# Kernel tuning notes

Hardware: AMD Instinct MI355X
Metric: run time of the kernel (lower is better)

## Reference

```python
import jax, jax.numpy as jnp
import numpy as np

N_SRC = 50000
N_DST = 10000
E = 1600000
H = 1
F = 128
NEG_SLOPE = 0.2  # GAT default leaky_relu slope


def setup_inputs() -> dict:
    key = jax.random.key(0)
    k1, k2, k3, k4, k5, k6 = jax.random.split(key, 6)
    x_src = jax.random.normal(k1, (N_SRC, H, F), dtype=jnp.float32)
    x_dst = jax.random.normal(k2, (N_DST, H, F), dtype=jnp.float32)
    attn_l = jax.random.normal(k3, (1, H, F), dtype=jnp.float32)
    attn_r = jax.random.normal(k4, (1, H, F), dtype=jnp.float32)
    src_idx = jax.random.randint(k5, (E,), 0, N_SRC, dtype=jnp.int64 if jax.config.jax_enable_x64 else jnp.int32)
    dst_idx = jnp.sort(jax.random.randint(k6, (E,), 0, N_DST, dtype=jnp.int64 if jax.config.jax_enable_x64 else jnp.int32))
    return {"x_src": x_src, "x_dst": x_dst, "attn_l": attn_l, "attn_r": attn_r,
            "src_idx": src_idx, "dst_idx": dst_idx}


def reference(x_src, x_dst, attn_l, attn_r, src_idx, dst_idx):
    n_dst = x_dst.shape[0]
    # per-node attention logits: [N, H]
    el = (x_src * attn_l).sum(axis=-1)
    er = (x_dst * attn_r).sum(axis=-1)
    # per-edge score e = leaky_relu(el[u] + er[v]): [E, H]
    e = jax.nn.leaky_relu(el[src_idx] + er[dst_idx], negative_slope=NEG_SLOPE)
    ex = jnp.exp(e)
    # segment-sum over destination neighborhoods: [N_dst, H]
    sum_ex = jax.ops.segment_sum(ex, dst_idx, num_segments=n_dst)
    attention = ex / sum_ex[dst_idx]  # [E, H]
    # attention-weighted gather of src features, scattered to dst: [N_dst, H, F]
    msg = attention[..., None] * x_src[src_idx]
    out = jax.ops.segment_sum(msg, dst_idx, num_segments=n_dst)
    return out
```

## Files before the change

### kernel.cpp

```cpp
#include <hip/hip_runtime.h>
#include <hip/hip_fp16.h>

#define F 128
#define NEG_SLOPE 0.2f
#define NB 8

__global__ __launch_bounds__(256)
void prep_kernel(const float* __restrict__ x_src, const float* __restrict__ attn_l,
                 float* __restrict__ el, __half2* __restrict__ xh, int n_src,
                 const float* __restrict__ x_dst, const float* __restrict__ attn_r,
                 float* __restrict__ er, int n_dst,
                 const int* __restrict__ dst_idx, int* __restrict__ offs, int E,
                 int nlog) {
    if ((int)blockIdx.x < nlog) {
        int row  = blockIdx.x * 4 + (threadIdx.x >> 6);
        int lane = threadIdx.x & 63;
        if (row < n_src) {
            float2 xv = *reinterpret_cast<const float2*>(&x_src[(size_t)row * F + lane * 2]);
            float2 av = *reinterpret_cast<const float2*>(&attn_l[lane * 2]);
            if (xh) xh[(size_t)row * (F / 2) + lane] = __floats2half2_rn(xv.x, xv.y);
            float s = xv.x * av.x + xv.y * av.y;
            #pragma unroll
            for (int o = 32; o > 0; o >>= 1) s += __shfl_xor(s, o, 64);
            if (lane == 0) el[row] = s;
        } else if (row < n_src + n_dst) {
            int r = row - n_src;
            float2 xv = *reinterpret_cast<const float2*>(&x_dst[(size_t)r * F + lane * 2]);
            float2 av = *reinterpret_cast<const float2*>(&attn_r[lane * 2]);
            float s = xv.x * av.x + xv.y * av.y;
            #pragma unroll
            for (int o = 32; o > 0; o >>= 1) s += __shfl_xor(s, o, 64);
            if (lane == 0) er[r] = s;
        }
    } else {
        int e = ((int)blockIdx.x - nlog) * 256 + threadIdx.x;
        if (e >= E) return;
        int d = dst_idx[e];
        int prev = (e == 0) ? -1 : dst_idx[e - 1];
        for (int v = prev + 1; v <= d; ++v) offs[v] = e;
        if (e == E - 1)
            for (int v = d + 1; v <= n_dst; ++v) offs[v] = E;
    }
}

__global__ __launch_bounds__(256)
void reorder_kernel(const int* __restrict__ src_idx, const int* __restrict__ offs,
                    int* __restrict__ src_r, int* __restrict__ boffs,
                    int n_dst, int bdiv) {
    int v   = blockIdx.x;
    int tid = threadIdx.x;
    int start = offs[v], end = offs[v + 1];

    __shared__ int cnt[NB];
    __shared__ int base_[NB];
    __shared__ int wtot[4];

    if (tid < NB) cnt[tid] = 0;
    __syncthreads();
    for (int i = start + tid; i < end; i += 256)
        atomicAdd(&cnt[src_idx[i] / bdiv], 1);
    __syncthreads();
    if (tid == 0) {
        int acc = start;
        #pragma unroll
        for (int b = 0; b < NB; ++b) {
            base_[b] = acc;
            boffs[(size_t)v * (NB + 1) + b] = acc;
            acc += cnt[b];
        }
        boffs[(size_t)v * (NB + 1) + NB] = acc;
    }
    __syncthreads();

    int lane = tid & 63, wid = tid >> 6;
    for (int cbase = start; cbase < end; cbase += 256) {
        int n = end - cbase; if (n > 256) n = 256;
        int s = 0, b = -1;
        if (tid < n) { s = src_idx[cbase + tid]; b = s / bdiv; }
        #pragma unroll
        for (int bb = 0; bb < NB; ++bb) {
            bool flag = (b == bb);
            unsigned long long m = __ballot(flag);
            int rk = __popcll(m & ((1ULL << lane) - 1ULL));
            if (lane == 0) wtot[wid] = __popcll(m);
            __syncthreads();
            int wpre = 0;
            for (int w = 0; w < wid; ++w) wpre += wtot[w];
            if (flag) src_r[base_[bb] + wpre + rk] = s;
            __syncthreads();
            if (tid == 0) base_[bb] += wtot[0] + wtot[1] + wtot[2] + wtot[3];
            __syncthreads();
        }
    }
}

__global__ __launch_bounds__(256)
void agg_slice_kernel(const __half2* __restrict__ xh,
                      const float* __restrict__ el,
                      const float* __restrict__ er,
                      const int* __restrict__ src_r,
                      const int* __restrict__ boffs,
                      float* __restrict__ part, float* __restrict__ pden,
                      int n_dst) {
    int b = blockIdx.x & (NB - 1);
    int v = (blockIdx.x >> 3) * 4 + (threadIdx.x >> 6);
    if (v >= n_dst) return;
    int lane = threadIdx.x & 63;
    int g    = lane >> 4;
    int l16  = lane & 15;

    int s0e = boffs[(size_t)v * (NB + 1) + b];
    int s1e = boffs[(size_t)v * (NB + 1) + b + 1];
    float erv = er[v];

    const float4* x4h = reinterpret_cast<const float4*>(xh);

    float a0[8], a1[8];
    #pragma unroll
    for (int k = 0; k < 8; ++k) { a0[k] = 0.f; a1[k] = 0.f; }
    float d0 = 0.f, d1 = 0.f;

    int count = s1e - s0e;
    int full  = count & ~7;
    for (int it = 0; it < full; it += 8) {
        int e0 = s0e + it + g;
        int e1 = e0 + 4;
        int s0 = src_r[e0];
        int s1 = src_r[e1];
        float l0 = el[s0] + erv, l1 = el[s1] + erv;
        l0 = l0 > 0.f ? l0 : NEG_SLOPE * l0;
        l1 = l1 > 0.f ? l1 : NEG_SLOPE * l1;
        float w0 = __expf(l0), w1 = __expf(l1);
        d0 += w0; d1 += w1;
        float4 r0 = x4h[(size_t)s0 * (F / 8) + l16];
        float4 r1 = x4h[(size_t)s1 * (F / 8) + l16];
        const __half2* h0 = reinterpret_cast<const __half2*>(&r0);
        const __half2* h1 = reinterpret_cast<const __half2*>(&r1);
        #pragma unroll
        for (int k = 0; k < 4; ++k) {
            float2 f0 = __half22float2(h0[k]);
            float2 f1 = __half22float2(h1[k]);
            a0[2*k]   += w0 * f0.x;  a0[2*k+1] += w0 * f0.y;
            a1[2*k]   += w1 * f1.x;  a1[2*k+1] += w1 * f1.y;
        }
    }
    for (int e = s0e + full + g; e < s1e; e += 4) {
        int s = src_r[e];
        float l = el[s] + erv;
        l = l > 0.f ? l : NEG_SLOPE * l;
        float w = __expf(l);
        d0 += w;
        float4 r = x4h[(size_t)s * (F / 8) + l16];
        const __half2* h = reinterpret_cast<const __half2*>(&r);
        #pragma unroll
        for (int k = 0; k < 4; ++k) {
            float2 f = __half22float2(h[k]);
            a0[2*k] += w * f.x;  a0[2*k+1] += w * f.y;
        }
    }
    #pragma unroll
    for (int k = 0; k < 8; ++k) a0[k] += a1[k];
    d0 += d1;

    #pragma unroll
    for (int k = 0; k < 8; ++k) {
        a0[k] += __shfl_xor(a0[k], 16, 64);
        a0[k] += __shfl_xor(a0[k], 32, 64);
    }
    d0 += __shfl_xor(d0, 16, 64);
    d0 += __shfl_xor(d0, 32, 64);

    if (g == 0) {
        float4* pp = reinterpret_cast<float4*>(&part[((size_t)b * n_dst + v) * F + l16 * 8]);
        pp[0] = make_float4(a0[0], a0[1], a0[2], a0[3]);
        pp[1] = make_float4(a0[4], a0[5], a0[6], a0[7]);
        if (l16 == 0) pden[(size_t)b * n_dst + v] = d0;
    }
}

__global__ __launch_bounds__(256)
void combine_kernel(const float* __restrict__ part, const float* __restrict__ pden,
                    float* __restrict__ out, int n_dst) {
    int t = blockIdx.x * 256 + threadIdx.x;
    if (t >= n_dst * F) return;
    int v = t >> 7;
    float num = 0.f, den = 0.f;
    #pragma unroll
    for (int b = 0; b < NB; ++b) {
        num += part[((size_t)b * n_dst) * F + t];
        den += pden[(size_t)b * n_dst + v];
    }
    out[t] = (den > 0.f) ? num / den : 0.f;
}

template<bool H>
__global__ __launch_bounds__(256)
void agg_full_kernel(const __half2* __restrict__ xh, const float* __restrict__ x_src,
                     const float* __restrict__ el, const float* __restrict__ er,
                     const int* __restrict__ src_idx, const int* __restrict__ offs,
                     float* __restrict__ out, int n_dst) {
    int v = blockIdx.x * 4 + (threadIdx.x >> 6);
    if (v >= n_dst) return;
    int lane = threadIdx.x & 63;
    int g    = lane >> 4;
    int l16  = lane & 15;

    int start = offs[v];
    int end   = offs[v + 1];
    int count = end - start;
    float erv = er[v];

    const float4* x4h = reinterpret_cast<const float4*>(xh);
    const float4* x4f = reinterpret_cast<const float4*>(x_src);

    float a0[8], a1[8];
    #pragma unroll
    for (int k = 0; k < 8; ++k) { a0[k] = 0.f; a1[k] = 0.f; }
    float d0 = 0.f, d1 = 0.f;

    int full = count & ~7;
    for (int it = 0; it < full; it += 8) {
        int e0 = start + it + g;
        int e1 = e0 + 4;
        int s0 = src_idx[e0];
        int s1 = src_idx[e1];
        float l0 = el[s0] + erv, l1 = el[s1] + erv;
        l0 = l0 > 0.f ? l0 : NEG_SLOPE * l0;
        l1 = l1 > 0.f ? l1 : NEG_SLOPE * l1;
        float w0 = __expf(l0), w1 = __expf(l1);
        d0 += w0; d1 += w1;
        if (H) {
            float4 r0 = x4h[(size_t)s0 * (F / 8) + l16];
            float4 r1 = x4h[(size_t)s1 * (F / 8) + l16];
            const __half2* h0 = reinterpret_cast<const __half2*>(&r0);
            const __half2* h1 = reinterpret_cast<const __half2*>(&r1);
            #pragma unroll
            for (int k = 0; k < 4; ++k) {
                float2 f0 = __half22float2(h0[k]);
                float2 f1 = __half22float2(h1[k]);
                a0[2*k]   += w0 * f0.x;  a0[2*k+1] += w0 * f0.y;
                a1[2*k]   += w1 * f1.x;  a1[2*k+1] += w1 * f1.y;
            }
        } else {
            float4 p0 = x4f[(size_t)s0 * (F/4) + l16*2];
            float4 q0 = x4f[(size_t)s0 * (F/4) + l16*2 + 1];
            float4 p1 = x4f[(size_t)s1 * (F/4) + l16*2];
            float4 q1 = x4f[(size_t)s1 * (F/4) + l16*2 + 1];
            a0[0]+=w0*p0.x; a0[1]+=w0*p0.y; a0[2]+=w0*p0.z; a0[3]+=w0*p0.w;
            a0[4]+=w0*q0.x; a0[5]+=w0*q0.y; a0[6]+=w0*q0.z; a0[7]+=w0*q0.w;
            a1[0]+=w1*p1.x; a1[1]+=w1*p1.y; a1[2]+=w1*p1.z; a1[3]+=w1*p1.w;
            a1[4]+=w1*q1.x; a1[5]+=w1*q1.y; a1[6]+=w1*q1.z; a1[7]+=w1*q1.w;
        }
    }
    for (int e = start + full + g; e < end; e += 4) {
        int s = src_idx[e];
        float l = el[s] + erv;
        l = l > 0.f ? l : NEG_SLOPE * l;
        float w = __expf(l);
        d0 += w;
        if (H) {
            float4 r = x4h[(size_t)s * (F / 8) + l16];
            const __half2* h = reinterpret_cast<const __half2*>(&r);
            #pragma unroll
            for (int k = 0; k < 4; ++k) {
                float2 f = __half22float2(h[k]);
                a0[2*k] += w * f.x;  a0[2*k+1] += w * f.y;
            }
        } else {
            float4 p = x4f[(size_t)s * (F/4) + l16*2];
            float4 q = x4f[(size_t)s * (F/4) + l16*2 + 1];
            a0[0]+=w*p.x; a0[1]+=w*p.y; a0[2]+=w*p.z; a0[3]+=w*p.w;
            a0[4]+=w*q.x; a0[5]+=w*q.y; a0[6]+=w*q.z; a0[7]+=w*q.w;
        }
    }
    #pragma unroll
    for (int k = 0; k < 8; ++k) a0[k] += a1[k];
    d0 += d1;

    #pragma unroll
    for (int k = 0; k < 8; ++k) {
        a0[k] += __shfl_xor(a0[k], 16, 64);
        a0[k] += __shfl_xor(a0[k], 32, 64);
    }
    d0 += __shfl_xor(d0, 16, 64);
    d0 += __shfl_xor(d0, 32, 64);

    if (g == 0) {
        float inv = (count > 0) ? 1.f / d0 : 0.f;
        float4* dst = reinterpret_cast<float4*>(&out[(size_t)v * F + l16 * 8]);
        dst[0] = make_float4(a0[0]*inv, a0[1]*inv, a0[2]*inv, a0[3]*inv);
        dst[1] = make_float4(a0[4]*inv, a0[5]*inv, a0[6]*inv, a0[7]*inv);
    }
}

extern "C" void kernel_launch(void* const* d_in, const int* in_sizes, int n_in,
                              void* d_out, int out_size, void* d_ws, size_t ws_size,
                              hipStream_t stream) {
    const float* x_src   = (const float*)d_in[0];
    const float* x_dst   = (const float*)d_in[1];
    const float* attn_l  = (const float*)d_in[2];
    const float* attn_r  = (const float*)d_in[3];
    const int*   src_idx = (const int*)d_in[4];
    const int*   dst_idx = (const int*)d_in[5];

    int n_src = in_sizes[0] / F;
    int n_dst = in_sizes[1] / F;
    int E     = in_sizes[4];

    float* out  = (float*)d_out;
    float* el   = (float*)d_ws;
    float* er   = el + n_src;
    int*   offs = (int*)(er + n_dst);
    uintptr_t p = (uintptr_t)(offs + n_dst + 1);
    p = (p + 15) & ~(uintptr_t)15;
    __half2* xh = (__half2*)p;
    uintptr_t q = p + (size_t)n_src * F * sizeof(__half);
    int*   src_r = (int*)q;
    int*   boffs = src_r + E;
    uintptr_t r  = (uintptr_t)(boffs + (size_t)n_dst * (NB + 1));
    r = (r + 15) & ~(uintptr_t)15;
    float* part  = (float*)r;
    float* pden  = part + (size_t)NB * n_dst * F;

    size_t need_fp16 = (p - (uintptr_t)d_ws) + (size_t)n_src * F * sizeof(__half);
    size_t need_full = ((uintptr_t)(pden + (size_t)NB * n_dst)) - (uintptr_t)d_ws;
    bool fp16ok = ws_size >= need_fp16;
    bool fullok = ws_size >= need_full;

    int nlog = (n_src + n_dst + 3) / 4;
    int noff = (E + 255) / 256;
    prep_kernel<<<nlog + noff, 256, 0, stream>>>(
        x_src, attn_l, el, fp16ok ? xh : nullptr, n_src,
        x_dst, attn_r, er, n_dst, dst_idx, offs, E, nlog);

    if (fullok && fp16ok) {
        int bdiv = (n_src + NB - 1) / NB;
        reorder_kernel<<<n_dst, 256, 0, stream>>>(src_idx, offs, src_r, boffs,
                                                  n_dst, bdiv);
        int ngrp = (n_dst + 3) / 4;
        agg_slice_kernel<<<ngrp * NB, 256, 0, stream>>>(
            xh, el, er, src_r, boffs, part, pden, n_dst);
        combine_kernel<<<(n_dst * F + 255) / 256, 256, 0, stream>>>(
            part, pden, out, n_dst);
    } else if (fp16ok) {
        agg_full_kernel<true><<<(n_dst + 3) / 4, 256, 0, stream>>>(
            xh, nullptr, el, er, src_idx, offs, out, n_dst);
    } else {
        agg_full_kernel<false><<<(n_dst + 3) / 4, 256, 0, stream>>>(
            nullptr, x_src, el, er, src_idx, offs, out, n_dst);
    }
}
```

Before: 90.42 us.

## Fuse edge weights into reorder, use wave-level binning, fma_mix, fewer slices

The reorder kernel now works one wavefront per destination with ballot-based binning and no block barriers. It also computes each edge's exp weight and writes a packed (row offset, weight) pair, so the aggregation kernel no longer gathers el or evaluates exp. The number of source slices drops from 8 to 4, which halves the partial buffers and the combine traffic. Other changes: v_fma_mix inline asm replaces the explicit half-to-float conversions, prep uses float4 loads with two rows per wave, and combine is vectorised to float4. Fewer slices means a larger gather working set per pass, and packing the weight doubles the bytes of the reordered edge array.

New measurement: 72.65 us, median of 3. 19.7% less time.

```diff
diff --git a/kernel.cpp b/kernel.cpp
--- a/kernel.cpp
+++ b/kernel.cpp
@@ -3,7 +3,14 @@
 
 #define F 128
 #define NEG_SLOPE 0.2f
-#define NB 8
+#define NB 4
+
+#define FMA_MIX_LO(acc, w, h) \
+    asm("v_fma_mix_f32 %0, %1, %2, %0 op_sel:[0,0,0] op_sel_hi:[0,1,0]" \
+        : "+v"(acc) : "v"(w), "v"(h))
+#define FMA_MIX_HI(acc, w, h) \
+    asm("v_fma_mix_f32 %0, %1, %2, %0 op_sel:[0,1,0] op_sel_hi:[0,1,0]" \
+        : "+v"(acc) : "v"(w), "v"(h))
 
 __global__ __launch_bounds__(256)
 void prep_kernel(const float* __restrict__ x_src, const float* __restrict__ attn_l,
@@ -13,25 +20,29 @@
                  const int* __restrict__ dst_idx, int* __restrict__ offs, int E,
                  int nlog) {
     if ((int)blockIdx.x < nlog) {
-        int row  = blockIdx.x * 4 + (threadIdx.x >> 6);
+        int wave = blockIdx.x * 4 + (threadIdx.x >> 6);
         int lane = threadIdx.x & 63;
-        if (row < n_src) {
-            float2 xv = *reinterpret_cast<const float2*>(&x_src[(size_t)row * F + lane * 2]);
-            float2 av = *reinterpret_cast<const float2*>(&attn_l[lane * 2]);
-            if (xh) xh[(size_t)row * (F / 2) + lane] = __floats2half2_rn(xv.x, xv.y);
-            float s = xv.x * av.x + xv.y * av.y;
-            #pragma unroll
-            for (int o = 32; o > 0; o >>= 1) s += __shfl_xor(s, o, 64);
-            if (lane == 0) el[row] = s;
-        } else if (row < n_src + n_dst) {
-            int r = row - n_src;
-            float2 xv = *reinterpret_cast<const float2*>(&x_dst[(size_t)r * F + lane * 2]);
-            float2 av = *reinterpret_cast<const float2*>(&attn_r[lane * 2]);
-            float s = xv.x * av.x + xv.y * av.y;
-            #pragma unroll
-            for (int o = 32; o > 0; o >>= 1) s += __shfl_xor(s, o, 64);
-            if (lane == 0) er[r] = s;
-        }
+        int half = lane >> 5;
+        int l32  = lane & 31;
+        int row  = wave * 2 + half;
+        const float* x; const float* attn; float* o; int r; bool is_src;
+        if (row < n_src)              { x = x_src; attn = attn_l; o = el; r = row; is_src = true; }
+        else if (row < n_src + n_dst) { x = x_dst; attn = attn_r; o = er; r = row - n_src; is_src = false; }
+        else return;
+        float4 xv = reinterpret_cast<const float4*>(x)[(size_t)r * 32 + l32];
+        float4 av = reinterpret_cast<const float4*>(attn)[l32];
+        if (xh && is_src) {
+            __half2 h0 = __floats2half2_rn(xv.x, xv.y);
+            __half2 h1 = __floats2half2_rn(xv.z, xv.w);
+            uint2 u;
+            u.x = *reinterpret_cast<unsigned int*>(&h0);
+            u.y = *reinterpret_cast<unsigned int*>(&h1);
+            reinterpret_cast<uint2*>(xh)[(size_t)r * 32 + l32] = u;
+        }
+        float s = xv.x * av.x + xv.y * av.y + xv.z * av.z + xv.w * av.w;
+        #pragma unroll
+        for (int o_ = 16; o_ > 0; o_ >>= 1) s += __shfl_xor(s, o_, 64);
+        if (l32 == 0) o[r] = s;
     } else {
         int e = ((int)blockIdx.x - nlog) * 256 + threadIdx.x;
         if (e >= E) return;
@@ -45,65 +56,79 @@
 
 __global__ __launch_bounds__(256)
 void reorder_kernel(const int* __restrict__ src_idx, const int* __restrict__ offs,
-                    int* __restrict__ src_r, int* __restrict__ boffs,
-                    int n_dst, int bdiv) {
-    int v   = blockIdx.x;
-    int tid = threadIdx.x;
+                    const float* __restrict__ el, const float* __restrict__ er,
+                    int2* __restrict__ ew, int* __restrict__ boffs,
+                    int n_dst, float inv_bdiv) {
+    int v = blockIdx.x * 4 + (threadIdx.x >> 6);
+    if (v >= n_dst) return;
+    int lane = threadIdx.x & 63;
     int start = offs[v], end = offs[v + 1];
-
-    __shared__ int cnt[NB];
-    __shared__ int base_[NB];
-    __shared__ int wtot[4];
-
-    if (tid < NB) cnt[tid] = 0;
-    __syncthreads();
-    for (int i = start + tid; i < end; i += 256)
-        atomicAdd(&cnt[src_idx[i] / bdiv], 1);
-    __syncthreads();
-    if (tid == 0) {
-        int acc = start;
-        #pragma unroll
-        for (int b = 0; b < NB; ++b) {
-            base_[b] = acc;
-            boffs[(size_t)v * (NB + 1) + b] = acc;
-            acc += cnt[b];
-        }
-        boffs[(size_t)v * (NB + 1) + NB] = acc;
-    }
-    __syncthreads();
-
-    int lane = tid & 63, wid = tid >> 6;
-    for (int cbase = start; cbase < end; cbase += 256) {
-        int n = end - cbase; if (n > 256) n = 256;
-        int s = 0, b = -1;
-        if (tid < n) { s = src_idx[cbase + tid]; b = s / bdiv; }
-        #pragma unroll
-        for (int bb = 0; bb < NB; ++bb) {
-            bool flag = (b == bb);
-            unsigned long long m = __ballot(flag);
-            int rk = __popcll(m & ((1ULL << lane) - 1ULL));
-            if (lane == 0) wtot[wid] = __popcll(m);
-            __syncthreads();
-            int wpre = 0;
-            for (int w = 0; w < wid; ++w) wpre += wtot[w];
-            if (flag) src_r[base_[bb] + wpre + rk] = s;
-            __syncthreads();
-            if (tid == 0) base_[bb] += wtot[0] + wtot[1] + wtot[2] + wtot[3];
-            __syncthreads();
-        }
+    float erv = er[v];
+    unsigned long long lt = (1ULL << lane) - 1ULL;
+
+    int c0 = 0, c1 = 0, c2 = 0, c3 = 0;
+    for (int base = start; base < end; base += 64) {
+        int e = base + lane;
+        int b = -1;
+        if (e < end) {
+            int s = src_idx[e];
+            b = (int)((float)s * inv_bdiv);
+            if (b > NB - 1) b = NB - 1;
+        }
+        c0 += __popcll(__ballot(b == 0));
+        c1 += __popcll(__ballot(b == 1));
+        c2 += __popcll(__ballot(b == 2));
+        c3 += __popcll(__ballot(b == 3));
+    }
+    int base0 = start;
+    int base1 = base0 + c0;
+    int base2 = base1 + c1;
+    int base3 = base2 + c2;
+    if (lane == 0) {
+        boffs[(size_t)v * (NB + 1) + 0] = base0;
+        boffs[(size_t)v * (NB + 1) + 1] = base1;
+        boffs[(size_t)v * (NB + 1) + 2] = base2;
+        boffs[(size_t)v * (NB + 1) + 3] = base3;
+        boffs[(size_t)v * (NB + 1) + 4] = base3 + c3;
+    }
+
+    for (int base = start; base < end; base += 64) {
+        int e = base + lane;
+        int b = -1, s = 0;
+        float w = 0.f;
+        if (e < end) {
+            s = src_idx[e];
+            b = (int)((float)s * inv_bdiv);
+            if (b > NB - 1) b = NB - 1;
+            float l = el[s] + erv;
+            l = l > 0.f ? l : NEG_SLOPE * l;
+            w = __expf(l);
+        }
+        int2 payload = make_int2(s * (F / 8), __float_as_int(w));
+        unsigned long long m;
+        m = __ballot(b == 0);
+        if (b == 0) ew[base0 + __popcll(m & lt)] = payload;
+        base0 += __popcll(m);
+        m = __ballot(b == 1);
+        if (b == 1) ew[base1 + __popcll(m & lt)] = payload;
+        base1 += __popcll(m);
+        m = __ballot(b == 2);
+        if (b == 2) ew[base2 + __popcll(m & lt)] = payload;
+        base2 += __popcll(m);
+        m = __ballot(b == 3);
+        if (b == 3) ew[base3 + __popcll(m & lt)] = payload;
+        base3 += __popcll(m);
     }
 }
 
 __global__ __launch_bounds__(256)
 void agg_slice_kernel(const __half2* __restrict__ xh,
-                      const float* __restrict__ el,
-                      const float* __restrict__ er,
-                      const int* __restrict__ src_r,
+                      const int2* __restrict__ ew,
                       const int* __restrict__ boffs,
                       float* __restrict__ part, float* __restrict__ pden,
                       int n_dst) {
     int b = blockIdx.x & (NB - 1);
-    int v = (blockIdx.x >> 3) * 4 + (threadIdx.x >> 6);
+    int v = ((int)blockIdx.x >> 2) * 4 + (threadIdx.x >> 6);
     if (v >= n_dst) return;
     int lane = threadIdx.x & 63;
     int g    = lane >> 4;
@@ -111,7 +136,6 @@
 
     int s0e = boffs[(size_t)v * (NB + 1) + b];
     int s1e = boffs[(size_t)v * (NB + 1) + b + 1];
-    float erv = er[v];
 
     const float4* x4h = reinterpret_cast<const float4*>(xh);
 
@@ -123,39 +147,33 @@
     int count = s1e - s0e;
     int full  = count & ~7;
     for (int it = 0; it < full; it += 8) {
-        int e0 = s0e + it + g;
-        int e1 = e0 + 4;
-        int s0 = src_r[e0];
-        int s1 = src_r[e1];
-        float l0 = el[s0] + erv, l1 = el[s1] + erv;
-        l0 = l0 > 0.f ? l0 : NEG_SLOPE * l0;
-        l1 = l1 > 0.f ? l1 : NEG_SLOPE * l1;
-        float w0 = __expf(l0), w1 = __expf(l1);
+        int2 q0 = ew[s0e + it + g];
+        int2 q1 = ew[s0e + it + 4 + g];
+        float w0 = __int_as_float(q0.y);
+        float w1 = __int_as_float(q1.y);
         d0 += w0; d1 += w1;
-        float4 r0 = x4h[(size_t)s0 * (F / 8) + l16];
-        float4 r1 = x4h[(size_t)s1 * (F / 8) + l16];
-        const __half2* h0 = reinterpret_cast<const __half2*>(&r0);
-        const __half2* h1 = reinterpret_cast<const __half2*>(&r1);
+        float4 r0 = x4h[q0.x + l16];
+        float4 r1 = x4h[q1.x + l16];
+        const unsigned int* u0 = reinterpret_cast<const unsigned int*>(&r0);
+        const unsigned int* u1 = reinterpret_cast<const unsigned int*>(&r1);
         #pragma unroll
         for (int k = 0; k < 4; ++k) {
-            float2 f0 = __half22float2(h0[k]);
-            float2 f1 = __half22float2(h1[k]);
-            a0[2*k]   += w0 * f0.x;  a0[2*k+1] += w0 * f0.y;
-            a1[2*k]   += w1 * f1.x;  a1[2*k+1] += w1 * f1.y;
+            FMA_MIX_LO(a0[2*k],   w0, u0[k]);
+            FMA_MIX_HI(a0[2*k+1], w0, u0[k]);
+            FMA_MIX_LO(a1[2*k],   w1, u1[k]);
+            FMA_MIX_HI(a1[2*k+1], w1, u1[k]);
         }
     }
     for (int e = s0e + full + g; e < s1e; e += 4) {
-        int s = src_r[e];
-        float l = el[s] + erv;
-        l = l > 0.f ? l : NEG_SLOPE * l;
-        float w = __expf(l);
+        int2 q = ew[e];
+        float w = __int_as_float(q.y);
         d0 += w;
-        float4 r = x4h[(size_t)s * (F / 8) + l16];
-        const __half2* h = reinterpret_cast<const __half2*>(&r);
+        float4 r = x4h[q.x + l16];
+        const unsigned int* u = reinterpret_cast<const unsigned int*>(&r);
         #pragma unroll
         for (int k = 0; k < 4; ++k) {
-            float2 f = __half22float2(h[k]);
-            a0[2*k] += w * f.x;  a0[2*k+1] += w * f.y;
+            FMA_MIX_LO(a0[2*k],   w, u[k]);
+            FMA_MIX_HI(a0[2*k+1], w, u[k]);
         }
     }
     #pragma unroll
@@ -182,15 +200,20 @@
 void combine_kernel(const float* __restrict__ part, const float* __restrict__ pden,
                     float* __restrict__ out, int n_dst) {
     int t = blockIdx.x * 256 + threadIdx.x;
-    if (t >= n_dst * F) return;
-    int v = t >> 7;
-    float num = 0.f, den = 0.f;
+    int total = n_dst * (F / 4);
+    if (t >= total) return;
+    int v = t >> 5;
+    const float4* p4 = reinterpret_cast<const float4*>(part);
+    float4 n = make_float4(0.f, 0.f, 0.f, 0.f);
+    float den = 0.f;
     #pragma unroll
     for (int b = 0; b < NB; ++b) {
-        num += part[((size_t)b * n_dst) * F + t];
+        float4 u = p4[(size_t)b * total + t];
+        n.x += u.x; n.y += u.y; n.z += u.z; n.w += u.w;
         den += pden[(size_t)b * n_dst + v];
     }
-    out[t] = (den > 0.f) ? num / den : 0.f;
+    float inv = (den > 0.f) ? 1.f / den : 0.f;
+    reinterpret_cast<float4*>(out)[t] = make_float4(n.x*inv, n.y*inv, n.z*inv, n.w*inv);
 }
 
 template<bool H>
@@ -213,46 +236,12 @@
     const float4* x4h = reinterpret_cast<const float4*>(xh);
     const float4* x4f = reinterpret_cast<const float4*>(x_src);
 
-    float a0[8], a1[8];
-    #pragma unroll
-    for (int k = 0; k < 8; ++k) { a0[k] = 0.f; a1[k] = 0.f; }
-    float d0 = 0.f, d1 = 0.f;
-
-    int full = count & ~7;
-    for (int it = 0; it < full; it += 8) {
-        int e0 = start + it + g;
-        int e1 = e0 + 4;
-        int s0 = src_idx[e0];
-        int s1 = src_idx[e1];
-        float l0 = el[s0] + erv, l1 = el[s1] + erv;
-        l0 = l0 > 0.f ? l0 : NEG_SLOPE * l0;
-        l1 = l1 > 0.f ? l1 : NEG_SLOPE * l1;
-        float w0 = __expf(l0), w1 = __expf(l1);
-        d0 += w0; d1 += w1;
-        if (H) {
-            float4 r0 = x4h[(size_t)s0 * (F / 8) + l16];
-            float4 r1 = x4h[(size_t)s1 * (F / 8) + l16];
-            const __half2* h0 = reinterpret_cast<const __half2*>(&r0);
-            const __half2* h1 = reinterpret_cast<const __half2*>(&r1);
-            #pragma unroll
-            for (int k = 0; k < 4; ++k) {
-                float2 f0 = __half22float2(h0[k]);
-                float2 f1 = __half22float2(h1[k]);
-                a0[2*k]   += w0 * f0.x;  a0[2*k+1] += w0 * f0.y;
-                a1[2*k]   += w1 * f1.x;  a1[2*k+1] += w1 * f1.y;
-            }
-        } else {
-            float4 p0 = x4f[(size_t)s0 * (F/4) + l16*2];
-            float4 q0 = x4f[(size_t)s0 * (F/4) + l16*2 + 1];
-            float4 p1 = x4f[(size_t)s1 * (F/4) + l16*2];
-            float4 q1 = x4f[(size_t)s1 * (F/4) + l16*2 + 1];
-            a0[0]+=w0*p0.x; a0[1]+=w0*p0.y; a0[2]+=w0*p0.z; a0[3]+=w0*p0.w;
-            a0[4]+=w0*q0.x; a0[5]+=w0*q0.y; a0[6]+=w0*q0.z; a0[7]+=w0*q0.w;
-            a1[0]+=w1*p1.x; a1[1]+=w1*p1.y; a1[2]+=w1*p1.z; a1[3]+=w1*p1.w;
-            a1[4]+=w1*q1.x; a1[5]+=w1*q1.y; a1[6]+=w1*q1.z; a1[7]+=w1*q1.w;
-        }
-    }
-    for (int e = start + full + g; e < end; e += 4) {
+    float a0[8];
+    #pragma unroll
+    for (int k = 0; k < 8; ++k) a0[k] = 0.f;
+    float d0 = 0.f;
+
+    for (int e = start + g; e < end; e += 4) {
         int s = src_idx[e];
         float l = el[s] + erv;
         l = l > 0.f ? l : NEG_SLOPE * l;
@@ -260,11 +249,11 @@
         d0 += w;
         if (H) {
             float4 r = x4h[(size_t)s * (F / 8) + l16];
-            const __half2* h = reinterpret_cast<const __half2*>(&r);
+            const unsigned int* u = reinterpret_cast<const unsigned int*>(&r);
             #pragma unroll
             for (int k = 0; k < 4; ++k) {
-                float2 f = __half22float2(h[k]);
-                a0[2*k] += w * f.x;  a0[2*k+1] += w * f.y;
+                FMA_MIX_LO(a0[2*k],   w, u[k]);
+                FMA_MIX_HI(a0[2*k+1], w, u[k]);
             }
         } else {
             float4 p = x4f[(size_t)s * (F/4) + l16*2];
@@ -273,10 +262,6 @@
             a0[4]+=w*q.x; a0[5]+=w*q.y; a0[6]+=w*q.z; a0[7]+=w*q.w;
         }
     }
-    #pragma unroll
-    for (int k = 0; k < 8; ++k) a0[k] += a1[k];
-    d0 += d1;
-
     #pragma unroll
     for (int k = 0; k < 8; ++k) {
         a0[k] += __shfl_xor(a0[k], 16, 64);
@@ -315,19 +300,20 @@
     p = (p + 15) & ~(uintptr_t)15;
     __half2* xh = (__half2*)p;
     uintptr_t q = p + (size_t)n_src * F * sizeof(__half);
-    int*   src_r = (int*)q;
-    int*   boffs = src_r + E;
+    q = (q + 15) & ~(uintptr_t)15;
+    int2*  ew    = (int2*)q;
+    int*   boffs = (int*)(ew + E);
     uintptr_t r  = (uintptr_t)(boffs + (size_t)n_dst * (NB + 1));
     r = (r + 15) & ~(uintptr_t)15;
     float* part  = (float*)r;
     float* pden  = part + (size_t)NB * n_dst * F;
 
-    size_t need_fp16 = (p - (uintptr_t)d_ws) + (size_t)n_src * F * sizeof(__half);
+    size_t need_fp16 = (q - (uintptr_t)d_ws);
     size_t need_full = ((uintptr_t)(pden + (size_t)NB * n_dst)) - (uintptr_t)d_ws;
     bool fp16ok = ws_size >= need_fp16;
     bool fullok = ws_size >= need_full;
 
-    int nlog = (n_src + n_dst + 3) / 4;
+    int nlog = (n_src + n_dst + 7) / 8;
     int noff = (E + 255) / 256;
     prep_kernel<<<nlog + noff, 256, 0, stream>>>(
         x_src, attn_l, el, fp16ok ? xh : nullptr, n_src,
@@ -335,12 +321,13 @@
 
     if (fullok && fp16ok) {
         int bdiv = (n_src + NB - 1) / NB;
-        reorder_kernel<<<n_dst, 256, 0, stream>>>(src_idx, offs, src_r, boffs,
-                                                  n_dst, bdiv);
+        float inv_bdiv = 1.0f / (float)bdiv;
+        reorder_kernel<<<(n_dst + 3) / 4, 256, 0, stream>>>(
+            src_idx, offs, el, er, ew, boffs, n_dst, inv_bdiv);
         int ngrp = (n_dst + 3) / 4;
         agg_slice_kernel<<<ngrp * NB, 256, 0, stream>>>(
-            xh, el, er, src_r, boffs, part, pden, n_dst);
-        combine_kernel<<<(n_dst * F + 255) / 256, 256, 0, stream>>>(
+            xh, ew, boffs, part, pden, n_dst);
+        combine_kernel<<<(n_dst * (F / 4) + 255) / 256, 256, 0, stream>>>(
             part, pden, out, n_dst);
     } else if (fp16ok) {
         agg_full_kernel<true><<<(n_dst + 3) / 4, 256, 0, stream>>>(
```
